# Kernel optimization log

Measured on AMD Instinct MI355X. Metric: run time of the kernel, lower is better.

Reference implementation:

```python
import jax, jax.numpy as jnp
import numpy as np

T, B, DIM, N_STATE = 2048, 16, 1024, 1024
EPS = 1e-6


def setup_inputs() -> dict:
    key = jax.random.key(0)
    kx, kk, kv, kq = jax.random.split(key, 4)
    xavier = np.sqrt(2.0 / (N_STATE + DIM)).astype(np.float32)
    return {
        "x": jax.random.normal(kx, (T, B, DIM), dtype=jnp.float32),
        "W_k": jax.random.normal(kk, (N_STATE, DIM), dtype=jnp.float32) * xavier,
        "W_v": jax.random.normal(kv, (N_STATE, DIM), dtype=jnp.float32) * xavier,
        "W_q": jax.random.normal(kq, (N_STATE, DIM), dtype=jnp.float32) * xavier,
    }


def reference(x, W_k, W_v, W_q):
    # Projections for all timesteps at once: [T, B, n]
    k = jnp.einsum("tbd,nd->tbn", x, W_k)
    v = jnp.einsum("tbd,nd->tbn", x, W_v)
    q = jnp.einsum("tbd,nd->tbn", x, W_q)
    # L2-normalize k per (t, b) over the state dim (matches k_t.norm(dim=-1))
    k_norm = k / (jnp.linalg.norm(k, axis=-1, keepdims=True) + EPS)

    Tn, Bn, n = k.shape
    S0 = jnp.zeros((Bn, n), dtype=x.dtype)

    def step(S, inp):
        k_t, v_t, q_t = inp
        # Delta update with OUTPUT gating + tanh nonlinearity
        S_new = jnp.tanh(S * (1.0 - k_t * k_t) + v_t * k_t)
        Sq = S_new * q_t
        out = Sq * jax.nn.silu(Sq)
        return S_new, out

    S_final, output = jax.lax.scan(step, S0, (k_norm, v, q))
    return output, S_final
```

## Files before the change

kernel.cpp:

```cpp
#include <hip/hip_runtime.h>
#include <hip/hip_fp16.h>

#define T_STEPS 2048
#define BATCH 16
#define DIMD 1024
#define NSTATE 1024
#define MROWS (T_STEPS * BATCH)
#define NCH (BATCH * NSTATE)

typedef _Float16 f16x8 __attribute__((ext_vector_type(8)));
typedef float f32x4 __attribute__((ext_vector_type(4)));

#define GAS(p) ((const __attribute__((address_space(1))) void*)(p))
#define LAS(p) ((__attribute__((address_space(3))) void*)(p))

__global__ void cvt_kernel(const float* __restrict__ src, _Float16* __restrict__ dst, int n8) {
  int i = blockIdx.x * blockDim.x + threadIdx.x;
  if (i >= n8) return;
  const float4* s4 = (const float4*)src;
  float4 a = s4[(size_t)i * 2];
  float4 b = s4[(size_t)i * 2 + 1];
  f16x8 o;
  o[0] = (_Float16)a.x; o[1] = (_Float16)a.y; o[2] = (_Float16)a.z; o[3] = (_Float16)a.w;
  o[4] = (_Float16)b.x; o[5] = (_Float16)b.y; o[6] = (_Float16)b.z; o[7] = (_Float16)b.w;
  *((f16x8*)dst + i) = o;
}

__global__ void cvtW_kernel(const float* __restrict__ wk, const float* __restrict__ wv,
                            const float* __restrict__ wq, _Float16* __restrict__ dst) {
  const float* src = blockIdx.y == 0 ? wk : blockIdx.y == 1 ? wv : wq;
  int i = blockIdx.x * blockDim.x + threadIdx.x;
  const float4* s4 = (const float4*)src;
  float4 a = s4[(size_t)i * 2];
  float4 b = s4[(size_t)i * 2 + 1];
  f16x8 o;
  o[0] = (_Float16)a.x; o[1] = (_Float16)a.y; o[2] = (_Float16)a.z; o[3] = (_Float16)a.w;
  o[4] = (_Float16)b.x; o[5] = (_Float16)b.y; o[6] = (_Float16)b.z; o[7] = (_Float16)b.w;
  *((f16x8*)dst + (size_t)blockIdx.y * (NSTATE * DIMD / 8) + i) = o;
}

__global__ __launch_bounds__(512, 1) void gemm_kernel(const _Float16* __restrict__ A,
                                                      const _Float16* __restrict__ Wcat,
                                                      _Float16* __restrict__ KVQt,
                                                      float* __restrict__ rnpart) {
  __shared__ _Float16 lds[65536];
  const int tid = threadIdx.x;
  const int lane = tid & 63;
  const int w = tid >> 6;
  const int wm = w >> 2;
  const int wn = w & 3;

  const int bid = blockIdx.x;
  const int swz = (bid & 7) * 192 + (bid >> 3);
  const int mat = swz >> 9;
  const int rem = swz & 511;
  const int tileM = rem >> 2;
  const int tileN = rem & 3;

  const _Float16* Ag = A + (size_t)tileM * 256 * DIMD;
  const _Float16* Bg = Wcat + (size_t)mat * NSTATE * DIMD + (size_t)tileN * 256 * DIMD;

  const int s0 = tid, s1 = tid + 512;
  const int sr0 = s0 >> 2, sc0 = ((s0 & 3) ^ ((s0 >> 3) & 3)) * 8;
  const int sr1 = s1 >> 2, sc1 = ((s1 & 3) ^ ((s1 >> 3) & 3)) * 8;

#define STAGE_H(G, buf, reg, TT, h)                                                     \
  do {                                                                                  \
    __builtin_amdgcn_global_load_lds(                                                   \
        GAS(G + (size_t)sr0 * DIMD + (TT) * 64 + (h) * 32 + sc0),                       \
        LAS(lds + (buf) * 32768 + (reg) * 8192 + s0 * 8), 16, 0, 0);                    \
    __builtin_amdgcn_global_load_lds(                                                   \
        GAS(G + (size_t)sr1 * DIMD + (TT) * 64 + (h) * 32 + sc1),                       \
        LAS(lds + (buf) * 32768 + (reg) * 8192 + s1 * 8), 16, 0, 0);                    \
  } while (0)

  f32x4 acc[8][4];
#pragma unroll
  for (int m = 0; m < 8; ++m)
#pragma unroll
    for (int n = 0; n < 4; ++n)
      acc[m][n] = (f32x4){0.f, 0.f, 0.f, 0.f};

  STAGE_H(Ag, 0, 0, 0, 0);
  STAGE_H(Bg, 0, 2, 0, 0);
  STAGE_H(Ag, 0, 1, 0, 1);
  STAGE_H(Bg, 0, 3, 0, 1);

  const int fr = lane & 15;
  const int cbp = ((lane >> 4) ^ ((fr >> 1) & 3)) * 8;

#define KTILE(T)                                                                        \
  do {                                                                                  \
    const int buf = (T) & 1, bufn = buf ^ 1;                                            \
    f16x8 a0[8], b0[4], a1[8], b1[4];                                                   \
                 \
    asm volatile("s_waitcnt vmcnt(4)" ::: "memory");                                    \
    __builtin_amdgcn_s_barrier();                                                       \
    __builtin_amdgcn_sched_barrier(0);                                                  \
    if ((T) + 1 < 16) STAGE_H(Ag, bufn, 0, (T) + 1, 0);                                 \
    _Pragma("unroll") for (int m = 0; m < 8; ++m)                                       \
        a0[m] = *(const f16x8*)(lds + buf * 32768 + 0 * 8192 +                          \
                                (wm * 128 + m * 16 + fr) * 32 + cbp);                   \
    _Pragma("unroll") for (int n = 0; n < 4; ++n)                                       \
        b0[n] = *(const f16x8*)(lds + buf * 32768 + 2 * 8192 +                          \
                                (wn * 64 + n * 16 + fr) * 32 + cbp);                    \
    __builtin_amdgcn_s_setprio(1);                                                      \
    _Pragma("unroll") for (int m = 0; m < 8; ++m) _Pragma("unroll") for (int n = 0; n < 2; ++n) \
        acc[m][n] = __builtin_amdgcn_mfma_f32_16x16x32_f16(a0[m], b0[n], acc[m][n], 0, 0, 0); \
    __builtin_amdgcn_s_setprio(0);                                                      \
                                         \
    if ((T) + 1 < 16) STAGE_H(Bg, bufn, 2, (T) + 1, 0);                                 \
    __builtin_amdgcn_s_setprio(1);                                                      \
    _Pragma("unroll") for (int m = 0; m < 8; ++m) _Pragma("unroll") for (int n = 2; n < 4; ++n) \
        acc[m][n] = __builtin_amdgcn_mfma_f32_16x16x32_f16(a0[m], b0[n], acc[m][n], 0, 0, 0); \
    __builtin_amdgcn_s_setprio(0);                                                      \
                  \
    if ((T) + 1 < 16) {                                                                 \
      asm volatile("s_waitcnt vmcnt(4)" ::: "memory");                                  \
    } else {                                                                            \
      asm volatile("s_waitcnt vmcnt(0)" ::: "memory");                                  \
    }                                                                                   \
    __builtin_amdgcn_s_barrier();                                                       \
    __builtin_amdgcn_sched_barrier(0);                                                  \
    if ((T) + 1 < 16) STAGE_H(Ag, bufn, 1, (T) + 1, 1);                                 \
    _Pragma("unroll") for (int m = 0; m < 8; ++m)                                       \
        a1[m] = *(const f16x8*)(lds + buf * 32768 + 1 * 8192 +                          \
                                (wm * 128 + m * 16 + fr) * 32 + cbp);                   \
    _Pragma("unroll") for (int n = 0; n < 4; ++n)                                       \
        b1[n] = *(const f16x8*)(lds + buf * 32768 + 3 * 8192 +                          \
                                (wn * 64 + n * 16 + fr) * 32 + cbp);                    \
    __builtin_amdgcn_s_setprio(1);                                                      \
    _Pragma("unroll") for (int m = 0; m < 8; ++m) _Pragma("unroll") for (int n = 0; n < 2; ++n) \
        acc[m][n] = __builtin_amdgcn_mfma_f32_16x16x32_f16(a1[m], b1[n], acc[m][n], 0, 0, 0); \
    __builtin_amdgcn_s_setprio(0);                                                      \
                                         \
    if ((T) + 1 < 16) STAGE_H(Bg, bufn, 3, (T) + 1, 1);                                 \
    __builtin_amdgcn_s_setprio(1);                                                      \
    _Pragma("unroll") for (int m = 0; m < 8; ++m) _Pragma("unroll") for (int n = 2; n < 4; ++n) \
        acc[m][n] = __builtin_amdgcn_mfma_f32_16x16x32_f16(a1[m], b1[n], acc[m][n], 0, 0, 0); \
    __builtin_amdgcn_s_setprio(0);                                                      \
  } while (0)

  KTILE(0);  KTILE(1);  KTILE(2);  KTILE(3);
  KTILE(4);  KTILE(5);  KTILE(6);  KTILE(7);
  KTILE(8);  KTILE(9);  KTILE(10); KTILE(11);
  KTILE(12); KTILE(13); KTILE(14); KTILE(15);

  const int cc = lane & 15;
  const int l4 = lane >> 4;
  _Float16* Cb = KVQt + (size_t)mat * ((size_t)MROWS * NSTATE) +
                 (size_t)(tileM * 2 + wm) * ((size_t)NCH * 8);
#pragma unroll
  for (int n = 0; n < 4; ++n)
#pragma unroll
    for (int j = 0; j < 4; ++j) {
      f16x8 pk;
#pragma unroll
      for (int m = 0; m < 8; ++m) pk[m] = (_Float16)acc[m][n][j];
      const int b = l4 * 4 + j;
      const int gcol = tileN * 256 + wn * 64 + n * 16 + cc;
      *(f16x8*)(Cb + ((size_t)(b * 1024 + gcol)) * 8) = pk;
    }

  if (mat == 0) {
#pragma unroll
    for (int m = 0; m < 8; ++m)
#pragma unroll
      for (int j = 0; j < 4; ++j) {
        float p = 0.f;
#pragma unroll
        for (int n = 0; n < 4; ++n) p += acc[m][n][j] * acc[m][n][j];
        p += __shfl_xor(p, 1);
        p += __shfl_xor(p, 2);
        p += __shfl_xor(p, 4);
        p += __shfl_xor(p, 8);
        if (cc == 0) {
          const int gr = tileM * 256 + wm * 128 + m * 16 + l4 * 4 + j;
          rnpart[(size_t)(tileN * 4 + wn) * MROWS + gr] = p;
        }
      }
  }
}

__global__ void rnfin_kernel(const float* __restrict__ part, float* __restrict__ rnT) {
  const int r = blockIdx.x * 256 + threadIdx.x;
  float s = 0.f;
#pragma unroll
  for (int i = 0; i < 16; ++i) s += part[(size_t)i * MROWS + r];
  rnT[(r & 15) * T_STEPS + (r >> 4)] = 1.f / (sqrtf(s) + 1e-6f);
}

#define STILE 16

#define LOADT(P, t0in)                                                        \
  do {                                                                        \
    const int tc = ((t0in) < T_STEPS) ? (t0in) : (T_STEPS - STILE);           \
    const size_t o0 = ((size_t)(tc >> 3) * NCH + c) * 8;                      \
    P##k0 = *(const f16x8*)(Kt + o0);                                         \
    P##k1 = *(const f16x8*)(Kt + o0 + (size_t)NCH * 8);                       \
    P##v0 = *(const f16x8*)(Vt + o0);                                         \
    P##v1 = *(const f16x8*)(Vt + o0 + (size_t)NCH * 8);                       \
    P##q0 = *(const f16x8*)(Qt + o0);                                         \
    P##q1 = *(const f16x8*)(Qt + o0 + (size_t)NCH * 8);                       \
    P##r0 = *(const f32x4*)(rnT + bb + tc);                                   \
    P##r1 = *(const f32x4*)(rnT + bb + tc + 4);                               \
    P##r2 = *(const f32x4*)(rnT + bb + tc + 8);                               \
    P##r3 = *(const f32x4*)(rnT + bb + tc + 12);                              \
  } while (0)

#define CHAINT(P)                                                             \
  do {                                                                        \
    float p2[STILE], m2[STILE];                                               \
    _Pragma("unroll") for (int i = 0; i < STILE; ++i) {                       \
      float kf = (float)((i < 8) ? P##k0[i & 7] : P##k1[i & 7]);              \
      float vf = (float)((i < 8) ? P##v0[i & 7] : P##v1[i & 7]);              \
      float rv = (i < 4) ? P##r0[i & 3]                                       \
               : (i < 8) ? P##r1[i & 3]                                       \
               : (i < 12) ? P##r2[i & 3] : P##r3[i & 3];                      \
      float kn = kf * rv;                                                     \
      float t = L2E2 * kn;                                                    \
      float a2 = fmaf(-t, kn, L2E2);                                          \
      float b2 = t * vf;                                                      \
      p2[i] = a2 + b2;                                                        \
      m2[i] = -2.f * a2;                                                      \
    }                                                                         \
    _Pragma("unroll") for (int i = 0; i < STILE; ++i) {                       \
      float u = fmaf(m2[i], r, p2[i]);                                        \
      float e = __builtin_amdgcn_exp2f(u);                                    \
      r = __builtin_amdgcn_rcpf(e + 1.f);                                     \
      Sv##P[i] = fmaf(-2.f, r, 1.f);                                          \
    }                                                                         \
  } while (0)

#define OUTT(P, t0)                                                           \
  do {                                                                        \
    _Pragma("unroll") for (int i = 0; i < STILE; ++i) {                       \
      float qf = (float)((i < 8) ? P##q0[i & 7] : P##q1[i & 7]);              \
      float z = Sv##P[i] * qf;                                                \
      float e = __builtin_amdgcn_exp2f(-L2E * z);                             \
      float sg = __builtin_amdgcn_rcpf(1.f + e);                              \
      out[(size_t)((t0) + i) * NCH + c] = (z * z) * sg;                       \
    }                                                                         \
  } while (0)

__global__ __launch_bounds__(64) void scan_kernel(const _Float16* __restrict__ Kt,
                                                  const _Float16* __restrict__ Vt,
                                                  const _Float16* __restrict__ Qt,
                                                  const float* __restrict__ rnT,
                                                  float* __restrict__ out,
                                                  float* __restrict__ sfin) {
  const int c = blockIdx.x * 64 + threadIdx.x;
  const int bb = (c >> 10) * T_STEPS;
  constexpr float L2E2 = 2.8853900817779268f;
  constexpr float L2E = 1.4426950408889634f;
  float r = 0.5f;
  f16x8 Ak0, Ak1, Av0, Av1, Aq0, Aq1;
  f16x8 Bk0, Bk1, Bv0, Bv1, Bq0, Bq1;
  f16x8 Ck0, Ck1, Cv0, Cv1, Cq0, Cq1;
  f32x4 Ar0, Ar1, Ar2, Ar3, Br0, Br1, Br2, Br3, Cr0, Cr1, Cr2, Cr3;
  float SvA[STILE], SvB[STILE], SvC[STILE];

  LOADT(A, 0);
  LOADT(B, STILE);
  CHAINT(A);
  LOADT(C, 2 * STILE);
  CHAINT(B);  OUTT(A, 0);
  LOADT(A, 3 * STILE);

  for (int t0 = 2 * STILE; t0 + 3 * STILE <= T_STEPS; t0 += 3 * STILE) {
    CHAINT(C);  OUTT(B, t0 - STILE);
    LOADT(B, t0 + 2 * STILE);
    CHAINT(A);  OUTT(C, t0);
    LOADT(C, t0 + 3 * STILE);
    CHAINT(B);  OUTT(A, t0 + STILE);
    LOADT(A, t0 + 4 * STILE);
  }
  OUTT(B, T_STEPS - STILE);
  sfin[c] = fmaf(-2.f, r, 1.f);
}

extern "C" void kernel_launch(void* const* d_in, const int* in_sizes, int n_in,
                              void* d_out, int out_size, void* d_ws, size_t ws_size,
                              hipStream_t stream) {
  const float* x = (const float*)d_in[0];
  const float* Wk = (const float*)d_in[1];
  const float* Wv = (const float*)d_in[2];
  const float* Wq = (const float*)d_in[3];

  char* ws = (char*)d_ws;
  _Float16* xh = (_Float16*)ws;
  _Float16* Wh = (_Float16*)(ws + 67108864ull);
  _Float16* KVQt = (_Float16*)(ws + 67108864ull + 6291456ull);
  float* rnpart = (float*)(ws + 67108864ull + 6291456ull + 201326592ull);
  float* rnT = (float*)(ws + 67108864ull + 6291456ull + 201326592ull + 2097152ull);

  int n8x = MROWS * DIMD / 8;
  cvt_kernel<<<(n8x + 255) / 256, 256, 0, stream>>>(x, xh, n8x);
  cvtW_kernel<<<dim3(NSTATE * DIMD / 8 / 256, 3), 256, 0, stream>>>(Wk, Wv, Wq, Wh);

  gemm_kernel<<<1536, 512, 0, stream>>>(xh, Wh, KVQt, rnpart);

  rnfin_kernel<<<MROWS / 256, 256, 0, stream>>>(rnpart, rnT);

  const _Float16* Kt = KVQt;
  const _Float16* Vt = KVQt + (size_t)MROWS * NSTATE;
  const _Float16* Qt = KVQt + 2ull * MROWS * NSTATE;
  float* outp = (float*)d_out;
  scan_kernel<<<NCH / 64, 64, 0, stream>>>(Kt, Vt, Qt, rnT, outp, outp + (size_t)MROWS * NSTATE);
}
```

Baseline: 389.3 us.

## Split scan into chain and output warps communicating through shared memory

The scan kernel now runs two wavefronts per block. One computes the serial tanh recurrence from K/V and writes states into a double-buffered shared-memory tile. The other loads Q, computes the gated output and writes it to global memory. The goal is to take the output math and stores off the latency-critical recurrence wavefront, at the cost of two block barriers per 32 steps and fewer register-held prefetch stages on the chain side.

```diff
diff --git a/kernel.cpp b/kernel.cpp
--- a/kernel.cpp
+++ b/kernel.cpp
@@ -192,7 +192,7 @@
 
 #define STILE 16
 
-#define LOADT(P, t0in)                                                        \
+#define LOADKV(P, t0in)                                                       \
   do {                                                                        \
     const int tc = ((t0in) < T_STEPS) ? (t0in) : (T_STEPS - STILE);           \
     const size_t o0 = ((size_t)(tc >> 3) * NCH + c) * 8;                      \
@@ -200,15 +200,21 @@
     P##k1 = *(const f16x8*)(Kt + o0 + (size_t)NCH * 8);                       \
     P##v0 = *(const f16x8*)(Vt + o0);                                         \
     P##v1 = *(const f16x8*)(Vt + o0 + (size_t)NCH * 8);                       \
-    P##q0 = *(const f16x8*)(Qt + o0);                                         \
-    P##q1 = *(const f16x8*)(Qt + o0 + (size_t)NCH * 8);                       \
     P##r0 = *(const f32x4*)(rnT + bb + tc);                                   \
     P##r1 = *(const f32x4*)(rnT + bb + tc + 4);                               \
     P##r2 = *(const f32x4*)(rnT + bb + tc + 8);                               \
     P##r3 = *(const f32x4*)(rnT + bb + tc + 12);                              \
   } while (0)
 
-#define CHAINT(P)                                                             \
+#define LOADQ(QP, t0in)                                                       \
+  do {                                                                        \
+    const int tc = ((t0in) < T_STEPS) ? (t0in) : (T_STEPS - STILE);           \
+    const size_t o0 = ((size_t)(tc >> 3) * NCH + c) * 8;                      \
+    QP##0 = *(const f16x8*)(Qt + o0);                                         \
+    QP##1 = *(const f16x8*)(Qt + o0 + (size_t)NCH * 8);                       \
+  } while (0)
+
+#define CHAINL(P, p)                                                          \
   do {                                                                        \
     float p2[STILE], m2[STILE];                                               \
     _Pragma("unroll") for (int i = 0; i < STILE; ++i) {                       \
@@ -220,63 +226,78 @@
       float kn = kf * rv;                                                     \
       float t = L2E2 * kn;                                                    \
       float a2 = fmaf(-t, kn, L2E2);                                          \
-      float b2 = t * vf;                                                      \
-      p2[i] = a2 + b2;                                                        \
+      p2[i] = a2 + t * vf;                                                    \
       m2[i] = -2.f * a2;                                                      \
     }                                                                         \
     _Pragma("unroll") for (int i = 0; i < STILE; ++i) {                       \
       float u = fmaf(m2[i], r, p2[i]);                                        \
       float e = __builtin_amdgcn_exp2f(u);                                    \
       r = __builtin_amdgcn_rcpf(e + 1.f);                                     \
-      Sv##P[i] = fmaf(-2.f, r, 1.f);                                          \
+      SvL[p][i][lane] = fmaf(-2.f, r, 1.f);                                   \
     }                                                                         \
   } while (0)
 
-#define OUTT(P, t0)                                                           \
+#define OUTL(QP, t0, p)                                                       \
   do {                                                                        \
     _Pragma("unroll") for (int i = 0; i < STILE; ++i) {                       \
-      float qf = (float)((i < 8) ? P##q0[i & 7] : P##q1[i & 7]);              \
-      float z = Sv##P[i] * qf;                                                \
+      float sv = SvL[p][i][lane];                                             \
+      float qf = (float)((i < 8) ? QP##0[i & 7] : QP##1[i & 7]);              \
+      float z = sv * qf;                                                      \
       float e = __builtin_amdgcn_exp2f(-L2E * z);                             \
       float sg = __builtin_amdgcn_rcpf(1.f + e);                              \
       out[(size_t)((t0) + i) * NCH + c] = (z * z) * sg;                       \
     }                                                                         \
   } while (0)
 
-__global__ __launch_bounds__(64) void scan_kernel(const _Float16* __restrict__ Kt,
-                                                  const _Float16* __restrict__ Vt,
-                                                  const _Float16* __restrict__ Qt,
-                                                  const float* __restrict__ rnT,
-                                                  float* __restrict__ out,
-                                                  float* __restrict__ sfin) {
-  const int c = blockIdx.x * 64 + threadIdx.x;
+__global__ __launch_bounds__(128) void scan_kernel(const _Float16* __restrict__ Kt,
+                                                   const _Float16* __restrict__ Vt,
+                                                   const _Float16* __restrict__ Qt,
+                                                   const float* __restrict__ rnT,
+                                                   float* __restrict__ out,
+                                                   float* __restrict__ sfin) {
+  __shared__ float SvL[2][STILE][64];
+  const int lane = threadIdx.x & 63;
+  const bool isChain = threadIdx.x < 64;
+  const int c = blockIdx.x * 64 + lane;
   const int bb = (c >> 10) * T_STEPS;
   constexpr float L2E2 = 2.8853900817779268f;
   constexpr float L2E = 1.4426950408889634f;
   float r = 0.5f;
-  f16x8 Ak0, Ak1, Av0, Av1, Aq0, Aq1;
-  f16x8 Bk0, Bk1, Bv0, Bv1, Bq0, Bq1;
-  f16x8 Ck0, Ck1, Cv0, Cv1, Cq0, Cq1;
-  f32x4 Ar0, Ar1, Ar2, Ar3, Br0, Br1, Br2, Br3, Cr0, Cr1, Cr2, Cr3;
-  float SvA[STILE], SvB[STILE], SvC[STILE];
-
-  LOADT(A, 0);
-  LOADT(B, STILE);
-  CHAINT(A);
-  LOADT(C, 2 * STILE);
-  CHAINT(B);  OUTT(A, 0);
-  LOADT(A, 3 * STILE);
-
-  for (int t0 = 2 * STILE; t0 + 3 * STILE <= T_STEPS; t0 += 3 * STILE) {
-    CHAINT(C);  OUTT(B, t0 - STILE);
-    LOADT(B, t0 + 2 * STILE);
-    CHAINT(A);  OUTT(C, t0);
-    LOADT(C, t0 + 3 * STILE);
-    CHAINT(B);  OUTT(A, t0 + STILE);
-    LOADT(A, t0 + 4 * STILE);
+  f16x8 Ak0, Ak1, Av0, Av1, Bk0, Bk1, Bv0, Bv1;
+  f32x4 Ar0, Ar1, Ar2, Ar3, Br0, Br1, Br2, Br3;
+  f16x8 Qe0, Qe1, Qo0, Qo1;
+
+  if (isChain) {
+    LOADKV(A, 0);
+    LOADKV(B, STILE);
+  } else {
+    LOADQ(Qe, 0);
   }
-  OUTT(B, T_STEPS - STILE);
-  sfin[c] = fmaf(-2.f, r, 1.f);
+
+  for (int j = 0; j < T_STEPS / 32; ++j) {
+    const int t0 = j * 32;
+    if (isChain) {
+      CHAINL(A, 0);
+      LOADKV(A, t0 + 2 * STILE);
+    } else {
+      if (j > 0) OUTL(Qo, t0 - STILE, 1);
+      LOADQ(Qo, t0 + STILE);
+    }
+    __syncthreads();
+    if (isChain) {
+      CHAINL(B, 1);
+      LOADKV(B, t0 + 3 * STILE);
+    } else {
+      OUTL(Qe, t0, 0);
+      LOADQ(Qe, t0 + 2 * STILE);
+    }
+    __syncthreads();
+  }
+  if (isChain) {
+    if (lane < 64) sfin[c] = fmaf(-2.f, r, 1.f);
+  } else {
+    OUTL(Qo, T_STEPS - STILE, 1);
+  }
 }
 
 extern "C" void kernel_launch(void* const* d_in, const int* in_sizes, int n_in,
@@ -306,5 +327,5 @@
   const _Float16* Vt = KVQt + (size_t)MROWS * NSTATE;
   const _Float16* Qt = KVQt + 2ull * MROWS * NSTATE;
   float* outp = (float*)d_out;
-  scan_kernel<<<NCH / 64, 64, 0, stream>>>(Kt, Vt, Qt, rnT, outp, outp + (size_t)MROWS * NSTATE);
-}
+  scan_kernel<<<NCH / 64, 128, 0, stream>>>(Kt, Vt, Qt, rnT, outp, outp + (size_t)MROWS * NSTATE);
+}
```

Result: faster. 376.7 us (-3.2%).
